# Optimization experiments

Hardware: AMD Instinct MI355X
Metric: run time of the kernel (lower is better)

The kernel has to match this reference:

```python
import jax, jax.numpy as jnp
import numpy as np

B = 16384      # number of batched 6-node FC graphs
A = 6          # num_agents (nodes per graph)
D_OBS = 128    # raw observation dim
D_EMB = 250    # embedding / GAT feature dim
H = 3          # GAT heads (head outputs averaged to keep dim 250)
HID = 256
N_ACT = 5
NEG_SLOPE = 0.2


def setup_inputs() -> dict:
    key = jax.random.key(0)
    ks = jax.random.split(key, 16)
    def w(i, shape, scale=0.05):
        return jax.random.normal(ks[i], shape, dtype=jnp.float32) * scale
    return {
        "x": jax.random.normal(ks[0], (B * A, D_OBS), dtype=jnp.float32),
        "W_emb": w(1, (D_OBS, D_EMB)), "b_emb": jnp.zeros((D_EMB,), jnp.float32),
        "W_gat": w(2, (H, D_EMB, D_EMB)),
        "a_l": w(3, (H, D_EMB)), "a_r": w(4, (H, D_EMB)),
        "W1": w(5, (2 * D_EMB, HID)), "b1": jnp.zeros((HID,), jnp.float32),
        "W2": w(6, (HID, N_ACT)), "b2": jnp.zeros((N_ACT,), jnp.float32),
        "V1": w(7, (2 * D_EMB, HID)), "vb1": jnp.zeros((HID,), jnp.float32),
        "V2": w(8, (HID, 1)), "vb2": jnp.zeros((1,), jnp.float32),
    }


def reference(x, W_emb, b_emb, W_gat, a_l, a_r, W1, b1, W2, b2, V1, vb1, V2, vb2):
    # embedding layer
    h = jax.nn.relu(x @ W_emb + b_emb)                       # [N, 250]
    hb = h.reshape(B, A, D_EMB)                              # [B, 6, 250]
    # GAT on fully-connected 6-node graphs (incl. self edges), dense-masked form
    Wh = jnp.einsum("bad,hde->bhae", hb, W_gat)              # [B, H, 6, 250]
    el = jnp.einsum("bhae,he->bha", Wh, a_l)                 # dst term
    er = jnp.einsum("bhae,he->bha", Wh, a_r)                 # src term
    e = jax.nn.leaky_relu(el[:, :, :, None] + er[:, :, None, :], NEG_SLOPE)  # [B,H,6,6]
    attn = jax.nn.softmax(e, axis=-1)                        # edge softmax over neighbors
    gat = jnp.einsum("bhij,bhje->bhie", attn, Wh).mean(axis=1)  # mean over heads -> [B,6,250]
    feat = jnp.concatenate([hb, gat], axis=-1).reshape(B * A, 2 * D_EMB)  # [N, 500]
    # actor head (reg1)
    probs = jax.nn.softmax(jax.nn.relu(feat @ W1 + b1) @ W2 + b2, axis=-1)  # [N, 5]
    # critic head (reg2)
    value = jax.nn.relu(feat @ V1 + vb1) @ V2 + vb2           # [N, 1]
    return jnp.concatenate([probs, value], axis=-1)          # [N, 6]
```

## Files before the change

### kernel.cpp

```cpp
#include <hip/hip_runtime.h>

typedef unsigned short u16;
typedef unsigned int   u32;
typedef unsigned long long u64;
typedef __attribute__((ext_vector_type(4))) int   i32x4;
typedef __attribute__((ext_vector_type(4))) float f32x4;
typedef __attribute__((ext_vector_type(8))) short s16x8;

#define NROWS 98304L
#define LDF   512

__device__ __forceinline__ u16 f2bf(float x) {
  union { float f; u32 u; } v; v.f = x;
  return (u16)((v.u + 0x7FFFu + ((v.u >> 16) & 1u)) >> 16);
}
__device__ __forceinline__ float bf2f(u16 b) {
  union { float f; u32 u; } v; v.u = ((u32)b) << 16;
  return v.f;
}

__device__ __forceinline__ void gload_lds16(const u16* g, u16* l) {
  __builtin_amdgcn_global_load_lds(
      (const __attribute__((address_space(1))) unsigned int*)g,
      (__attribute__((address_space(3))) unsigned int*)l, 16, 0, 0);
}

__global__ __launch_bounds__(256)
void prep_weights(const float* __restrict__ W_emb, const float* __restrict__ b_emb,
                  const float* __restrict__ W_gat, const float* __restrict__ a_l,
                  const float* __restrict__ a_r, const float* __restrict__ W1,
                  const float* __restrict__ b1, const float* __restrict__ V1,
                  const float* __restrict__ vb1,
                  u16* __restrict__ Wemb_t, u16* __restrict__ Wgat_t,
                  u16* __restrict__ W1V1_t, float* __restrict__ bembp,
                  float* __restrict__ b1vb1)
{
  const int idx = blockIdx.x * 256 + threadIdx.x;
  const int stride = gridDim.x * 256;
  for (int t = idx; t < 256 * 128; t += stride) {
    int n = t >> 7, k = t & 127;
    Wemb_t[t] = f2bf(n < 250 ? W_emb[k * 250 + n] : 0.f);
  }
  for (int t = idx; t < 3 * 256 * 256; t += stride) {
    int h = t >> 16, rem = t & 65535, e = rem >> 8, d = rem & 255;
    float v = 0.f;
    if (e < 250 && d < 250) {
      v = W_gat[(h * 250 + d) * 250 + e];
    } else if ((e == 250 || e == 251) && d < 250) {
      const float* av = ((e == 250) ? a_l : a_r) + h * 250;
      const float* wrow = W_gat + ((long)h * 250 + d) * 250;
      float s = 0.f;
      for (int q = 0; q < 250; q++) s += wrow[q] * av[q];
      v = s;
    }
    Wgat_t[t] = f2bf(v);
  }
  for (int t = idx; t < 512 * 512; t += stride) {
    int n = t >> 9, k = t & 511;
    const float* src = (n < 256) ? W1 : V1;
    int col = n & 255;
    float v = 0.f;
    if (k < 250) v = src[k * 256 + col];
    else if (k >= 256 && k < 506) v = src[(k - 6) * 256 + col];
    W1V1_t[t] = f2bf(v);
  }
  for (int t = idx; t < 512; t += stride) b1vb1[t] = (t < 256) ? b1[t] : vb1[t - 256];
  for (int t = idx; t < 256; t += stride) bembp[t] = (t < 250) ? b_emb[t] : 0.f;
}

__global__ __launch_bounds__(256, 2)
void gemm1f(const float* __restrict__ X,
            const u16* __restrict__ B,
            u16* __restrict__ C,
            const float* __restrict__ bias)
{
  __shared__ __align__(16) u16 At[128 * 64];
  __shared__ __align__(16) u16 Bt[128 * 64];
  const int tid = threadIdx.x;
  const int w = tid >> 6, lane = tid & 63;
  const int fl = lane & 15, fh = lane >> 4;
  const int wr = (w >> 1) * 64, wc = (w & 1) * 64;
  const int srow = lane >> 3;
  const int slot = lane & 7;
  const int schunk = ((slot ^ srow) << 3);
  const int swz = (fl & 7) << 3;

  const int nidx = blockIdx.x;
  const int midx = blockIdx.y;

  const float* Ax = X + (long)midx * 128 * 128;
  const u16* Bb = B + nidx * 128 * 128;
  u16* Cb = C + (long)midx * 128 * LDF + nidx * 128;
  const float* biasb = bias + nidx * 128;

  f32x4 acc[4][4];
  #pragma unroll
  for (int m = 0; m < 4; m++)
    #pragma unroll
    for (int n = 0; n < 4; n++)
      acc[m][n] = f32x4{0.f, 0.f, 0.f, 0.f};

  for (int ks = 0; ks < 2; ks++) {
    __syncthreads();
    #pragma unroll
    for (int c = 0; c < 4; c++) {
      const int row = w * 32 + c * 8 + srow;
      gload_lds16(Bb + (long)row * 128 + ks * 64 + schunk, Bt + (w * 4 + c) * 512);
      const float* src = Ax + (long)row * 128 + ks * 64 + schunk;
      f32x4 lo = *(const f32x4*)src;
      f32x4 hi = *(const f32x4*)(src + 4);
      i32x4 o;
      o[0] = (int)((u32)f2bf(lo[0]) | ((u32)f2bf(lo[1]) << 16));
      o[1] = (int)((u32)f2bf(lo[2]) | ((u32)f2bf(lo[3]) << 16));
      o[2] = (int)((u32)f2bf(hi[0]) | ((u32)f2bf(hi[1]) << 16));
      o[3] = (int)((u32)f2bf(hi[2]) | ((u32)f2bf(hi[3]) << 16));
      *(i32x4*)(At + row * 64 + slot * 8) = o;
    }
    __syncthreads();
    #pragma unroll
    for (int kk = 0; kk < 2; kk++) {
      s16x8 af[4], bfr[4];
      #pragma unroll
      for (int m = 0; m < 4; m++)
        af[m] = *(const s16x8*)(At + (wr + m * 16 + fl) * 64 + ((kk * 32 + fh * 8) ^ swz));
      #pragma unroll
      for (int n = 0; n < 4; n++)
        bfr[n] = *(const s16x8*)(Bt + (wc + n * 16 + fl) * 64 + ((kk * 32 + fh * 8) ^ swz));
      #pragma unroll
      for (int m = 0; m < 4; m++)
        #pragma unroll
        for (int n = 0; n < 4; n++)
          acc[m][n] = __builtin_amdgcn_mfma_f32_16x16x32_bf16(af[m], bfr[n], acc[m][n], 0, 0, 0);
    }
  }
  #pragma unroll
  for (int m = 0; m < 4; m++) {
    const int r0 = wr + m * 16 + fh * 4;
    #pragma unroll
    for (int n = 0; n < 4; n++) {
      const int col = wc + n * 16 + fl;
      const float bvv = biasb[col];
      f32x4 v = acc[m][n];
      #pragma unroll
      for (int r = 0; r < 4; r++)
        Cb[(long)(r0 + r) * LDF + col] = f2bf(fmaxf(v[r] + bvv, 0.f));
    }
  }
}

template<int KSTEPS>
__global__ __launch_bounds__(256, 2)
void gemm_bf16(const u16* __restrict__ A, int lda,
               const u16* __restrict__ B, int ldb, long strideB,
               u16* __restrict__ C, int ldc, long strideC, int nb)
{
  __shared__ __align__(16) u16 At[128 * 64];
  __shared__ __align__(16) u16 Bt[128 * 64];
  const int tid = threadIdx.x;
  const int w = tid >> 6, lane = tid & 63;
  const int fl = lane & 15, fh = lane >> 4;
  const int wr = (w >> 1) * 64, wc = (w & 1) * 64;
  const int srow = lane >> 3;
  const int scol = (((lane & 7) ^ srow) << 3);
  const int swz = (fl & 7) << 3;

  const int nidx = blockIdx.x % nb;
  const int zidx = blockIdx.x / nb;
  const int midx = blockIdx.y;

  const u16* Ab = A + (long)midx * 128 * lda;
  const u16* Bb = B + (long)zidx * strideB + (long)nidx * 128 * ldb;
  u16* Cb = C + (long)zidx * strideC + (long)midx * 128 * ldc + nidx * 128;

  f32x4 acc[4][4];
  #pragma unroll
  for (int m = 0; m < 4; m++)
    #pragma unroll
    for (int n = 0; n < 4; n++)
      acc[m][n] = f32x4{0.f, 0.f, 0.f, 0.f};

  for (int ks = 0; ks < KSTEPS; ks++) {
    __syncthreads();
    #pragma unroll
    for (int c = 0; c < 4; c++) {
      const int row = w * 32 + c * 8 + srow;
      gload_lds16(Ab + (long)row * lda + ks * 64 + scol, At + (w * 4 + c) * 512);
      gload_lds16(Bb + (long)row * ldb + ks * 64 + scol, Bt + (w * 4 + c) * 512);
    }
    __syncthreads();
    #pragma unroll
    for (int kk = 0; kk < 2; kk++) {
      s16x8 af[4], bfr[4];
      #pragma unroll
      for (int m = 0; m < 4; m++)
        af[m] = *(const s16x8*)(At + (wr + m * 16 + fl) * 64 + ((kk * 32 + fh * 8) ^ swz));
      #pragma unroll
      for (int n = 0; n < 4; n++)
        bfr[n] = *(const s16x8*)(Bt + (wc + n * 16 + fl) * 64 + ((kk * 32 + fh * 8) ^ swz));
      #pragma unroll
      for (int m = 0; m < 4; m++)
        #pragma unroll
        for (int n = 0; n < 4; n++)
          acc[m][n] = __builtin_amdgcn_mfma_f32_16x16x32_bf16(af[m], bfr[n], acc[m][n], 0, 0, 0);
    }
  }
  #pragma unroll
  for (int m = 0; m < 4; m++) {
    const int r0 = wr + m * 16 + fh * 4;
    #pragma unroll
    for (int n = 0; n < 4; n++) {
      const int col = wc + n * 16 + fl;
      f32x4 v = acc[m][n];
      #pragma unroll
      for (int r = 0; r < 4; r++)
        Cb[(long)(r0 + r) * ldc + col] = f2bf(v[r]);
    }
  }
}

__global__ __launch_bounds__(256, 4)
void gemm3p(const u16* __restrict__ A,
            const u16* __restrict__ B,
            const float* __restrict__ b1vb1,
            const float* __restrict__ W2,
            const float* __restrict__ V2,
            float* __restrict__ partials)
{
  __shared__ __align__(16) u16 At[128 * 64];
  __shared__ __align__(16) u16 Bt[128 * 64];
  __shared__ float pstage[2][128][6];
  const int tid = threadIdx.x;
  const int w = tid >> 6, lane = tid & 63;
  const int fl = lane & 15, fh = lane >> 4;
  const int wr = (w >> 1) * 64, wc = (w & 1) * 64;
  const int wcid = w & 1;
  const int srow = lane >> 3;
  const int scol = (((lane & 7) ^ srow) << 3);
  const int swz = (fl & 7) << 3;

  const int midx = blockIdx.x;
  const int nidx = blockIdx.y;

  const u16* Ab = A + (long)midx * 128 * 512;
  const u16* Bb = B + (long)nidx * 128 * 512;

  f32x4 acc[4][4];
  #pragma unroll
  for (int m = 0; m < 4; m++)
    #pragma unroll
    for (int n = 0; n < 4; n++)
      acc[m][n] = f32x4{0.f, 0.f, 0.f, 0.f};

  for (int ks = 0; ks < 8; ks++) {
    __syncthreads();
    #pragma unroll
    for (int c = 0; c < 4; c++) {
      const int row = w * 32 + c * 8 + srow;
      gload_lds16(Ab + (long)row * 512 + ks * 64 + scol, At + (w * 4 + c) * 512);
      gload_lds16(Bb + (long)row * 512 + ks * 64 + scol, Bt + (w * 4 + c) * 512);
    }
    __syncthreads();
    #pragma unroll
    for (int kk = 0; kk < 2; kk++) {
      s16x8 af[4], bfr[4];
      #pragma unroll
      for (int m = 0; m < 4; m++)
        af[m] = *(const s16x8*)(At + (wr + m * 16 + fl) * 64 + ((kk * 32 + fh * 8) ^ swz));
      #pragma unroll
      for (int n = 0; n < 4; n++)
        bfr[n] = *(const s16x8*)(Bt + (wc + n * 16 + fl) * 64 + ((kk * 32 + fh * 8) ^ swz));
      #pragma unroll
      for (int m = 0; m < 4; m++)
        #pragma unroll
        for (int n = 0; n < 4; n++)
          acc[m][n] = __builtin_amdgcn_mfma_f32_16x16x32_bf16(af[m], bfr[n], acc[m][n], 0, 0, 0);
    }
  }

  float bv[4];
  #pragma unroll
  for (int n = 0; n < 4; n++) bv[n] = b1vb1[nidx * 128 + wc + n * 16 + fl];

  #pragma unroll
  for (int m = 0; m < 4; m++) {
    float hidv[4][4];
    #pragma unroll
    for (int n = 0; n < 4; n++)
      #pragma unroll
      for (int r = 0; r < 4; r++)
        hidv[n][r] = fmaxf(acc[m][n][r] + bv[n], 0.f);
    const int row0 = wr + m * 16 + fh * 4;

    if (nidx < 2) {
      #pragma unroll
      for (int j = 0; j < 5; j++) {
        float ps[4] = {0.f, 0.f, 0.f, 0.f};
        #pragma unroll
        for (int n = 0; n < 4; n++) {
          const float w2 = W2[(nidx * 128 + wc + n * 16 + fl) * 5 + j];
          #pragma unroll
          for (int r = 0; r < 4; r++) ps[r] += hidv[n][r] * w2;
        }
        #pragma unroll
        for (int off = 1; off < 16; off <<= 1)
          #pragma unroll
          for (int r = 0; r < 4; r++) ps[r] += __shfl_xor(ps[r], off, 16);
        if (fl == 0) {
          #pragma unroll
          for (int r = 0; r < 4; r++) pstage[wcid][row0 + r][j] = ps[r];
        }
      }
    } else {
      float ps[4] = {0.f, 0.f, 0.f, 0.f};
      #pragma unroll
      for (int n = 0; n < 4; n++) {
        const float v2c = V2[nidx * 128 + wc + n * 16 + fl - 256];
        #pragma unroll
        for (int r = 0; r < 4; r++) ps[r] += hidv[n][r] * v2c;
      }
      #pragma unroll
      for (int off = 1; off < 16; off <<= 1)
        #pragma unroll
        for (int r = 0; r < 4; r++) ps[r] += __shfl_xor(ps[r], off, 16);
      if (fl == 0) {
        #pragma unroll
        for (int r = 0; r < 4; r++) pstage[wcid][row0 + r][5] = ps[r];
      }
    }
  }
  __syncthreads();

  if (tid < 128) {
    float* dst = partials + ((long)nidx * NROWS + (long)midx * 128 + tid) * 6;
    if (nidx < 2) {
      #pragma unroll
      for (int j = 0; j < 5; j++)
        dst[j] = pstage[0][tid][j] + pstage[1][tid][j];
    } else {
      dst[5] = pstage[0][tid][5] + pstage[1][tid][5];
    }
  }
}

__global__ __launch_bounds__(256)
void heads_final(const float* __restrict__ partials, const float* __restrict__ b2,
                 const float* __restrict__ vb2, float* __restrict__ out)
{
  const long row = (long)blockIdx.x * 256 + threadIdx.x;
  const long slab = NROWS * 6;
  const float* p = partials + row * 6;
  float lg[5];
  #pragma unroll
  for (int j = 0; j < 5; j++) lg[j] = p[j] + p[slab + j] + b2[j];
  const float val = p[2 * slab + 5] + p[3 * slab + 5] + vb2[0];
  float mx = -1e30f;
  #pragma unroll
  for (int j = 0; j < 5; j++) mx = fmaxf(mx, lg[j]);
  float s = 0.f, e[5];
  #pragma unroll
  for (int j = 0; j < 5; j++) { e[j] = __expf(lg[j] - mx); s += e[j]; }
  const float inv = 1.f / s;
  float* op = out + row * 6;
  #pragma unroll
  for (int j = 0; j < 5; j++) op[j] = e[j] * inv;
  op[5] = val;
}

__global__ __launch_bounds__(256)
void attn_gat(const u16* __restrict__ Wh, u16* __restrict__ feat)
{
  const int w = threadIdx.x >> 6, lane = threadIdx.x & 63;
  const long g = (long)blockIdx.x * 4 + w;
  const int c0 = lane * 4;

  u64 raw[3][6];
  #pragma unroll
  for (int h = 0; h < 3; h++)
    #pragma unroll
    for (int i = 0; i < 6; i++)
      raw[h][i] = *(const u64*)(Wh + (((long)h * NROWS + g * 6 + i) << 8) + c0);

  float gacc[6][4];
  #pragma unroll
  for (int i = 0; i < 6; i++)
    #pragma unroll
    for (int q = 0; q < 4; q++) gacc[i][q] = 0.f;

  #pragma unroll
  for (int h = 0; h < 3; h++) {
    float whf[6][4];
    #pragma unroll
    for (int i = 0; i < 6; i++) {
      u64 v = raw[h][i];
      whf[i][0] = bf2f((u16)v);
      whf[i][1] = bf2f((u16)(v >> 16));
      whf[i][2] = bf2f((u16)(v >> 32));
      whf[i][3] = bf2f((u16)(v >> 48));
    }
    float el[6], er[6];
    #pragma unroll
    for (int i = 0; i < 6; i++) {
      el[i] = __shfl(whf[i][2], 62, 64);
      er[i] = __shfl(whf[i][3], 62, 64);
    }
    #pragma unroll
    for (int i = 0; i < 6; i++) {
      float e[6]; float mx = -1e30f;
      #pragma unroll
      for (int j = 0; j < 6; j++) {
        float t = el[i] + er[j];
        t = (t > 0.f) ? t : 0.2f * t;
        e[j] = t; mx = fmaxf(mx, t);
      }
      float s = 0.f;
      #pragma unroll
      for (int j = 0; j < 6; j++) { e[j] = __expf(e[j] - mx); s += e[j]; }
      float inv = 1.f / s;
      #pragma unroll
      for (int j = 0; j < 6; j++) {
        float a = e[j] * inv;
        #pragma unroll
        for (int q = 0; q < 4; q++) gacc[i][q] += a * whf[j][q];
      }
    }
  }
  #pragma unroll
  for (int i = 0; i < 6; i++) {
    const float k = 1.f / 3.f;
    u64 o = (u64)f2bf(gacc[i][0] * k)
          | ((u64)f2bf(gacc[i][1] * k) << 16)
          | ((u64)f2bf(gacc[i][2] * k) << 32)
          | ((u64)f2bf(gacc[i][3] * k) << 48);
    *(u64*)(feat + (g * 6 + i) * LDF + 256 + c0) = o;
  }
}

extern "C" void kernel_launch(void* const* d_in, const int* in_sizes, int n_in,
                              void* d_out, int out_size, void* d_ws, size_t ws_size,
                              hipStream_t stream)
{
  const float* x     = (const float*)d_in[0];
  const float* W_emb = (const float*)d_in[1];
  const float* b_emb = (const float*)d_in[2];
  const float* W_gat = (const float*)d_in[3];
  const float* a_l   = (const float*)d_in[4];
  const float* a_r   = (const float*)d_in[5];
  const float* W1    = (const float*)d_in[6];
  const float* b1    = (const float*)d_in[7];
  const float* W2    = (const float*)d_in[8];
  const float* b2    = (const float*)d_in[9];
  const float* V1    = (const float*)d_in[10];
  const float* vb1   = (const float*)d_in[11];
  const float* V2    = (const float*)d_in[12];
  const float* vb2   = (const float*)d_in[13];

  char* ws = (char*)d_ws;
  u16* feat = (u16*)ws;
  char* r2  = ws + 100663296L;
  u16*   Whb      = (u16*)r2;
  float* partials = (float*)r2;
  char* wt  = r2 + 150994944L;
  u16*   Wemb_t = (u16*)wt;
  u16*   Wgat_t = (u16*)(wt + 65536);
  u16*   W1V1_t = (u16*)(wt + 458752);
  float* b1vb1  = (float*)(wt + 983040);
  float* bembp  = (float*)(wt + 985088);

  prep_weights<<<256, 256, 0, stream>>>(W_emb, b_emb, W_gat, a_l, a_r, W1, b1, V1, vb1,
                                        Wemb_t, Wgat_t, W1V1_t, bembp, b1vb1);
  gemm1f<<<dim3(2, 768), 256, 0, stream>>>(x, Wemb_t, feat, bembp);
  gemm_bf16<4><<<dim3(6, 768), 256, 0, stream>>>(feat, 512, Wgat_t, 256, 65536L,
                                                 Whb, 256, 25165824L, 2);
  attn_gat<<<4096, 256, 0, stream>>>(Whb, feat);
  gemm3p<<<dim3(768, 4), 256, 0, stream>>>(feat, W1V1_t, b1vb1, W2, V2, partials);
  heads_final<<<384, 256, 0, stream>>>(partials, b2, vb2, (float*)d_out);
}
```

Before: 352.0 us.

## Fuse GAT projection GEMM with attention softmax aggregation in one kernel

Replaces the separate Wh GEMM and attention kernel with one kernel. Each 512-thread block computes Wh for 48 rows (8 graphs) per head via MFMA and stages it in swizzled LDS. It then does the edge softmax and weighted aggregation on chip, which removes the round trip of the large Wh intermediate through global memory and one launch. In exchange each block reloads the full 256x256 W_gat slice per head and only has an M-tile of 48, so MFMA utilisation per block is lower and LDS use is larger.

After: 382.1 us. +8.6%, slower.

```diff
diff --git a/kernel.cpp b/kernel.cpp
--- a/kernel.cpp
+++ b/kernel.cpp
@@ -148,73 +148,139 @@
   }
 }
 
-template<int KSTEPS>
-__global__ __launch_bounds__(256, 2)
-void gemm_bf16(const u16* __restrict__ A, int lda,
-               const u16* __restrict__ B, int ldb, long strideB,
-               u16* __restrict__ C, int ldc, long strideC, int nb)
-{
-  __shared__ __align__(16) u16 At[128 * 64];
-  __shared__ __align__(16) u16 Bt[128 * 64];
+__global__ __launch_bounds__(512, 4)
+void gat_fused(const u16* __restrict__ feat_in,
+               const u16* __restrict__ Wg,
+               u16* __restrict__ feat_out)
+{
+  __shared__ __align__(16) u16 At[48 * 64];
+  __shared__ __align__(16) u16 Bt[256 * 64];
+  __shared__ __align__(16) u16 stash[48 * 256];
   const int tid = threadIdx.x;
   const int w = tid >> 6, lane = tid & 63;
   const int fl = lane & 15, fh = lane >> 4;
-  const int wr = (w >> 1) * 64, wc = (w & 1) * 64;
+  const int wc = w * 32;
   const int srow = lane >> 3;
-  const int scol = (((lane & 7) ^ srow) << 3);
+  const int slot = lane & 7;
+  const int schunk = ((slot ^ srow) << 3);
   const int swz = (fl & 7) << 3;
 
-  const int nidx = blockIdx.x % nb;
-  const int zidx = blockIdx.x / nb;
-  const int midx = blockIdx.y;
-
-  const u16* Ab = A + (long)midx * 128 * lda;
-  const u16* Bb = B + (long)zidx * strideB + (long)nidx * 128 * ldb;
-  u16* Cb = C + (long)zidx * strideC + (long)midx * 128 * ldc + nidx * 128;
-
-  f32x4 acc[4][4];
-  #pragma unroll
-  for (int m = 0; m < 4; m++)
-    #pragma unroll
-    for (int n = 0; n < 4; n++)
-      acc[m][n] = f32x4{0.f, 0.f, 0.f, 0.f};
-
-  for (int ks = 0; ks < KSTEPS; ks++) {
-    __syncthreads();
-    #pragma unroll
-    for (int c = 0; c < 4; c++) {
-      const int row = w * 32 + c * 8 + srow;
-      gload_lds16(Ab + (long)row * lda + ks * 64 + scol, At + (w * 4 + c) * 512);
-      gload_lds16(Bb + (long)row * ldb + ks * 64 + scol, Bt + (w * 4 + c) * 512);
-    }
-    __syncthreads();
-    #pragma unroll
-    for (int kk = 0; kk < 2; kk++) {
-      s16x8 af[4], bfr[4];
-      #pragma unroll
-      for (int m = 0; m < 4; m++)
-        af[m] = *(const s16x8*)(At + (wr + m * 16 + fl) * 64 + ((kk * 32 + fh * 8) ^ swz));
-      #pragma unroll
-      for (int n = 0; n < 4; n++)
-        bfr[n] = *(const s16x8*)(Bt + (wc + n * 16 + fl) * 64 + ((kk * 32 + fh * 8) ^ swz));
-      #pragma unroll
-      for (int m = 0; m < 4; m++)
-        #pragma unroll
-        for (int n = 0; n < 4; n++)
-          acc[m][n] = __builtin_amdgcn_mfma_f32_16x16x32_bf16(af[m], bfr[n], acc[m][n], 0, 0, 0);
-    }
-  }
-  #pragma unroll
-  for (int m = 0; m < 4; m++) {
-    const int r0 = wr + m * 16 + fh * 4;
-    #pragma unroll
-    for (int n = 0; n < 4; n++) {
-      const int col = wc + n * 16 + fl;
-      f32x4 v = acc[m][n];
-      #pragma unroll
-      for (int r = 0; r < 4; r++)
-        Cb[(long)(r0 + r) * ldc + col] = f2bf(v[r]);
-    }
+  const long rowbase = (long)blockIdx.x * 48;
+  const u16* Ab = feat_in + rowbase * LDF;
+
+  const int g = tid >> 6;
+  const int c0 = (lane) * 4;
+
+  float gacc[6][4];
+  #pragma unroll
+  for (int i = 0; i < 6; i++)
+    #pragma unroll
+    for (int q = 0; q < 4; q++) gacc[i][q] = 0.f;
+
+  for (int h = 0; h < 3; h++) {
+    const u16* Bb = Wg + h * 65536;
+    f32x4 acc[3][2];
+    #pragma unroll
+    for (int m = 0; m < 3; m++)
+      #pragma unroll
+      for (int n = 0; n < 2; n++) acc[m][n] = f32x4{0.f, 0.f, 0.f, 0.f};
+
+    for (int ks = 0; ks < 4; ks++) {
+      __syncthreads();
+      #pragma unroll
+      for (int s = 0; s < 4; s++) {
+        const int row = s * 64 + w * 8 + srow;
+        gload_lds16(Bb + (long)row * 256 + ks * 64 + schunk, Bt + (s * 64 + w * 8) * 64);
+      }
+      if (w < 6) {
+        const int row = w * 8 + srow;
+        gload_lds16(Ab + (long)row * LDF + ks * 64 + schunk, At + (w * 8) * 64);
+      }
+      __syncthreads();
+      #pragma unroll
+      for (int kk = 0; kk < 2; kk++) {
+        s16x8 af[3], bfr[2];
+        #pragma unroll
+        for (int m = 0; m < 3; m++)
+          af[m] = *(const s16x8*)(At + (m * 16 + fl) * 64 + ((kk * 32 + fh * 8) ^ swz));
+        #pragma unroll
+        for (int n = 0; n < 2; n++)
+          bfr[n] = *(const s16x8*)(Bt + (wc + n * 16 + fl) * 64 + ((kk * 32 + fh * 8) ^ swz));
+        #pragma unroll
+        for (int m = 0; m < 3; m++)
+          #pragma unroll
+          for (int n = 0; n < 2; n++)
+            acc[m][n] = __builtin_amdgcn_mfma_f32_16x16x32_bf16(af[m], bfr[n], acc[m][n], 0, 0, 0);
+      }
+    }
+    #pragma unroll
+    for (int m = 0; m < 3; m++)
+      #pragma unroll
+      for (int n = 0; n < 2; n++)
+        #pragma unroll
+        for (int r = 0; r < 4; r++) {
+          const int row = m * 16 + fh * 4 + r;
+          const int col = wc + n * 16 + fl;
+          const int byte = row * 512 + ((col * 2) ^ ((row & 7) << 4));
+          *(u16*)((char*)stash + byte) = f2bf(acc[m][n][r]);
+        }
+    __syncthreads();
+
+    float el[6], er[6], mx[6], inv[6];
+    #pragma unroll
+    for (int i = 0; i < 6; i++) {
+      const int row = g * 6 + i;
+      const int byte = row * 512 + (500 ^ ((row & 7) << 4));
+      const u32 v = *(const u32*)((const char*)stash + byte);
+      el[i] = bf2f((u16)v); er[i] = bf2f((u16)(v >> 16));
+    }
+    #pragma unroll
+    for (int i = 0; i < 6; i++) {
+      float m2 = -1e30f;
+      #pragma unroll
+      for (int j = 0; j < 6; j++) {
+        float t = el[i] + er[j];
+        t = (t > 0.f) ? t : 0.2f * t;
+        m2 = fmaxf(m2, t);
+      }
+      float s = 0.f;
+      #pragma unroll
+      for (int j = 0; j < 6; j++) {
+        float t = el[i] + er[j];
+        t = (t > 0.f) ? t : 0.2f * t;
+        s += __expf(t - m2);
+      }
+      mx[i] = m2; inv[i] = 1.f / s;
+    }
+    #pragma unroll
+    for (int j = 0; j < 6; j++) {
+      const int row = g * 6 + j;
+      const int byte = row * 512 + ((c0 * 2) ^ ((row & 7) << 4));
+      const u64 v = *(const u64*)((const char*)stash + byte);
+      float vj[4];
+      vj[0] = bf2f((u16)v);         vj[1] = bf2f((u16)(v >> 16));
+      vj[2] = bf2f((u16)(v >> 32)); vj[3] = bf2f((u16)(v >> 48));
+      const float erj = er[j];
+      #pragma unroll
+      for (int i = 0; i < 6; i++) {
+        float t = el[i] + erj;
+        t = (t > 0.f) ? t : 0.2f * t;
+        const float a = __expf(t - mx[i]) * inv[i];
+        #pragma unroll
+        for (int q = 0; q < 4; q++) gacc[i][q] += a * vj[q];
+      }
+    }
+    __syncthreads();
+  }
+
+  const float k3 = 1.f / 3.f;
+  #pragma unroll
+  for (int i = 0; i < 6; i++) {
+    u64 o = (u64)f2bf(gacc[i][0] * k3)
+          | ((u64)f2bf(gacc[i][1] * k3) << 16)
+          | ((u64)f2bf(gacc[i][2] * k3) << 32)
+          | ((u64)f2bf(gacc[i][3] * k3) << 48);
+    *(u64*)(feat_out + (rowbase + g * 6 + i) * LDF + 256 + c0) = o;
   }
 }
 
@@ -364,75 +430,6 @@
   #pragma unroll
   for (int j = 0; j < 5; j++) op[j] = e[j] * inv;
   op[5] = val;
-}
-
-__global__ __launch_bounds__(256)
-void attn_gat(const u16* __restrict__ Wh, u16* __restrict__ feat)
-{
-  const int w = threadIdx.x >> 6, lane = threadIdx.x & 63;
-  const long g = (long)blockIdx.x * 4 + w;
-  const int c0 = lane * 4;
-
-  u64 raw[3][6];
-  #pragma unroll
-  for (int h = 0; h < 3; h++)
-    #pragma unroll
-    for (int i = 0; i < 6; i++)
-      raw[h][i] = *(const u64*)(Wh + (((long)h * NROWS + g * 6 + i) << 8) + c0);
-
-  float gacc[6][4];
-  #pragma unroll
-  for (int i = 0; i < 6; i++)
-    #pragma unroll
-    for (int q = 0; q < 4; q++) gacc[i][q] = 0.f;
-
-  #pragma unroll
-  for (int h = 0; h < 3; h++) {
-    float whf[6][4];
-    #pragma unroll
-    for (int i = 0; i < 6; i++) {
-      u64 v = raw[h][i];
-      whf[i][0] = bf2f((u16)v);
-      whf[i][1] = bf2f((u16)(v >> 16));
-      whf[i][2] = bf2f((u16)(v >> 32));
-      whf[i][3] = bf2f((u16)(v >> 48));
-    }
-    float el[6], er[6];
-    #pragma unroll
-    for (int i = 0; i < 6; i++) {
-      el[i] = __shfl(whf[i][2], 62, 64);
-      er[i] = __shfl(whf[i][3], 62, 64);
-    }
-    #pragma unroll
-    for (int i = 0; i < 6; i++) {
-      float e[6]; float mx = -1e30f;
-      #pragma unroll
-      for (int j = 0; j < 6; j++) {
-        float t = el[i] + er[j];
-        t = (t > 0.f) ? t : 0.2f * t;
-        e[j] = t; mx = fmaxf(mx, t);
-      }
-      float s = 0.f;
-      #pragma unroll
-      for (int j = 0; j < 6; j++) { e[j] = __expf(e[j] - mx); s += e[j]; }
-      float inv = 1.f / s;
-      #pragma unroll
-      for (int j = 0; j < 6; j++) {
-        float a = e[j] * inv;
-        #pragma unroll
-        for (int q = 0; q < 4; q++) gacc[i][q] += a * whf[j][q];
-      }
-    }
-  }
-  #pragma unroll
-  for (int i = 0; i < 6; i++) {
-    const float k = 1.f / 3.f;
-    u64 o = (u64)f2bf(gacc[i][0] * k)
-          | ((u64)f2bf(gacc[i][1] * k) << 16)
-          | ((u64)f2bf(gacc[i][2] * k) << 32)
-          | ((u64)f2bf(gacc[i][3] * k) << 48);
-    *(u64*)(feat + (g * 6 + i) * LDF + 256 + c0) = o;
-  }
 }
 
 extern "C" void kernel_launch(void* const* d_in, const int* in_sizes, int n_in,
@@ -457,7 +454,6 @@
   char* ws = (char*)d_ws;
   u16* feat = (u16*)ws;
   char* r2  = ws + 100663296L;
-  u16*   Whb      = (u16*)r2;
   float* partials = (float*)r2;
   char* wt  = r2 + 150994944L;
   u16*   Wemb_t = (u16*)wt;
@@ -469,9 +465,7 @@
   prep_weights<<<256, 256, 0, stream>>>(W_emb, b_emb, W_gat, a_l, a_r, W1, b1, V1, vb1,
                                         Wemb_t, Wgat_t, W1V1_t, bembp, b1vb1);
   gemm1f<<<dim3(2, 768), 256, 0, stream>>>(x, Wemb_t, feat, bembp);
-  gemm_bf16<4><<<dim3(6, 768), 256, 0, stream>>>(feat, 512, Wgat_t, 256, 65536L,
-                                                 Whb, 256, 25165824L, 2);
-  attn_gat<<<4096, 256, 0, stream>>>(Whb, feat);
+  gat_fused<<<2048, 512, 0, stream>>>(feat, Wgat_t, feat);
   gemm3p<<<dim3(768, 4), 256, 0, stream>>>(feat, W1V1_t, b1vb1, W2, V2, partials);
   heads_final<<<384, 256, 0, stream>>>(partials, b2, vb2, (float*)d_out);
 }
```
